# Kernel optimization log

Measured on AMD Instinct MI355X. Metric: run time of the kernel, lower is better.

Reference implementation:

```python
import jax, jax.numpy as jnp
import numpy as np

BN_EPS = 1e-5


def setup_inputs() -> dict:
    key = jax.random.key(0)
    ks = jax.random.split(key, 12)
    N, K, C_IN, C_OUT = 50000, 16, 128, 128
    C2 = 2 * C_OUT
    return {
        "features": jax.random.normal(ks[0], (N, C_IN), dtype=jnp.float32),
        "neighbor_idx": jax.random.randint(ks[1], (N, K), 0, N, dtype=jnp.int64),
        "W1": jax.random.normal(ks[2], (C_IN, C2), dtype=jnp.float32) * 0.05,
        "b1": jax.random.normal(ks[3], (C2,), dtype=jnp.float32) * 0.05,
        "gamma": jax.random.uniform(ks[4], (C2,), dtype=jnp.float32, minval=0.5, maxval=1.5),
        "beta": jax.random.normal(ks[5], (C2,), dtype=jnp.float32) * 0.05,
        "run_mean": jax.random.normal(ks[6], (C2,), dtype=jnp.float32) * 0.05,
        "run_var": jax.random.uniform(ks[7], (C2,), dtype=jnp.float32, minval=0.5, maxval=1.5),
        "Ws": jax.random.normal(ks[8], (C2, C2), dtype=jnp.float32) * 0.05,
        "Wm": jax.random.normal(ks[9], (C2, C_OUT), dtype=jnp.float32) * 0.05,
        "bm": jax.random.normal(ks[10], (C_OUT,), dtype=jnp.float32) * 0.05,
    }


def reference(features, neighbor_idx, W1, b1, gamma, beta, run_mean, run_var, Ws, Wm, bm):
    # mlp1: Linear + ReLU (no BN)
    x = jax.nn.relu(features @ W1 + b1)                     # (N, 2C)
    # gather_neighbour: irregular index_select
    g = x[neighbor_idx]                                     # (N, k, 2C)
    # BatchNorm1d over channel dim (inference semantics, running stats)
    inv = gamma * jax.lax.rsqrt(run_var + BN_EPS)
    g = (g - run_mean) * inv + beta                         # (N, k, 2C)
    # AttentivePooling: per-neighbor score linear (no bias), softmax over k
    scores = jax.nn.softmax(g @ Ws, axis=1)                 # (N, k, 2C)
    feat = jnp.sum(scores * g, axis=1)                      # (N, 2C)
    return feat @ Wm + bm                                   # (N, C_out)
```

## Files before the change

kernel.cpp:

```cpp
#include <hip/hip_runtime.h>
#include <cstddef>

#define C_IN  128
#define C2    256
#define C_OUT 128
#define KNBR  16

typedef unsigned short u16;
typedef __attribute__((ext_vector_type(8))) short bf16x8;
typedef __attribute__((ext_vector_type(4))) float f32x4;

__device__ __forceinline__ float bf2f(u16 h) {
    return __uint_as_float(((unsigned int)h) << 16);
}
__device__ __forceinline__ u16 f2bf(float x) {
    unsigned int u = __float_as_uint(x);
    return (u16)((u + 0x7fffu + ((u >> 16) & 1u)) >> 16);
}

__global__ void prep_k(const float* __restrict__ W1, const float* __restrict__ Ws,
                       const float* __restrict__ Wm, u16* __restrict__ W1t,
                       u16* __restrict__ Wst, u16* __restrict__ Wmt)
{
    const int n = blockIdx.x, t = threadIdx.x;
    if (blockIdx.y == 0) {
        if (t < 128) W1t[n * 128 + t] = f2bf(W1[t * 256 + n]);
    } else if (blockIdx.y == 1) {
        Wst[n * 256 + t] = f2bf(Ws[t * 256 + n]);
    } else {
        if (n < 128) Wmt[n * 256 + t] = f2bf(Wm[t * 128 + n]);
    }
}

__global__ __launch_bounds__(256)
void mlp_k(const float* __restrict__ F, const u16* __restrict__ W1t,
           const u16* __restrict__ Wst,
           const float* __restrict__ bias, const float* __restrict__ gamma,
           const float* __restrict__ beta, const float* __restrict__ mean,
           const float* __restrict__ var,
           u16* __restrict__ packed, int N)
{
    __shared__ u16 As[128][136];
    __shared__ u16 Bs[128][72];
    __shared__ u16 xs[128][264];

    const int tid = threadIdx.x;
    const int w = tid >> 6, l = tid & 63, q = l >> 4, r = l & 15;
    const int wm = w & 1, wn = w >> 1;
    const int m0 = blockIdx.x * 128;

    #pragma unroll
    for (int i = 0; i < 16; i++) {
        int idx = tid + i * 256;
        int row = idx >> 5, c4 = (idx & 31) * 4;
        int gm = m0 + row;
        float4 v = make_float4(0.f, 0.f, 0.f, 0.f);
        if (gm < N) v = *(const float4*)(F + (size_t)gm * C_IN + c4);
        ushort4 h;
        h.x = f2bf(v.x); h.y = f2bf(v.y); h.z = f2bf(v.z); h.w = f2bf(v.w);
        *(ushort4*)&As[row][c4] = h;
    }

    #pragma unroll 1
    for (int nh = 0; nh < 2; nh++) {
        f32x4 acc[4][4] = {};
        #pragma unroll 1
        for (int k0 = 0; k0 < C_IN; k0 += 64) {
            __syncthreads();
            #pragma unroll
            for (int i = 0; i < 4; i++) {
                int idx = tid + i * 256;
                int row = idx >> 3, g = (idx & 7) * 8;
                *(uint4*)&Bs[row][g] = *(const uint4*)(
                    W1t + (size_t)(nh * 128 + row) * C_IN + k0 + g);
            }
            __syncthreads();
            #pragma unroll
            for (int h = 0; h < 2; h++) {
                bf16x8 af[4], bfr[4];
                #pragma unroll
                for (int i = 0; i < 4; i++)
                    af[i] = *(const bf16x8*)&As[wm * 64 + i * 16 + r][k0 + h * 32 + q * 8];
                #pragma unroll
                for (int j = 0; j < 4; j++)
                    bfr[j] = *(const bf16x8*)&Bs[wn * 64 + j * 16 + r][h * 32 + q * 8];
                #pragma unroll
                for (int i = 0; i < 4; i++)
                    #pragma unroll
                    for (int j = 0; j < 4; j++)
                        acc[i][j] = __builtin_amdgcn_mfma_f32_16x16x32_bf16(
                            af[i], bfr[j], acc[i][j], 0, 0, 0);
            }
        }
        #pragma unroll
        for (int j = 0; j < 4; j++) {
            const int ch = nh * 128 + wn * 64 + j * 16 + r;
            const float bi = bias[ch], be = beta[ch], mu = mean[ch];
            const float iv = gamma[ch] * rsqrtf(var[ch] + 1e-5f);
            #pragma unroll
            for (int i = 0; i < 4; i++) {
                const int mb = wm * 64 + i * 16 + q * 4;
                #pragma unroll
                for (int p = 0; p < 4; p++) {
                    const int ml = mb + p;
                    float x = fmaxf(acc[i][j][p] + bi, 0.f);
                    x = (x - mu) * iv + be;
                    u16 hx = f2bf(x);
                    xs[ml][ch] = hx;
                    if (m0 + ml < N)
                        packed[(size_t)(m0 + ml) * 512 + 256 + ch] = hx;
                }
            }
        }
    }

    #pragma unroll 1
    for (int nh = 0; nh < 2; nh++) {
        f32x4 acc[4][4] = {};
        #pragma unroll 1
        for (int k0 = 0; k0 < C2; k0 += 64) {
            __syncthreads();
            #pragma unroll
            for (int i = 0; i < 4; i++) {
                int idx = tid + i * 256;
                int row = idx >> 3, g = (idx & 7) * 8;
                *(uint4*)&Bs[row][g] = *(const uint4*)(
                    Wst + (size_t)(nh * 128 + row) * C2 + k0 + g);
            }
            __syncthreads();
            #pragma unroll
            for (int h = 0; h < 2; h++) {
                bf16x8 af[4], bfr[4];
                #pragma unroll
                for (int i = 0; i < 4; i++)
                    af[i] = *(const bf16x8*)&xs[wm * 64 + i * 16 + r][k0 + h * 32 + q * 8];
                #pragma unroll
                for (int j = 0; j < 4; j++)
                    bfr[j] = *(const bf16x8*)&Bs[wn * 64 + j * 16 + r][h * 32 + q * 8];
                #pragma unroll
                for (int i = 0; i < 4; i++)
                    #pragma unroll
                    for (int j = 0; j < 4; j++)
                        acc[i][j] = __builtin_amdgcn_mfma_f32_16x16x32_bf16(
                            af[i], bfr[j], acc[i][j], 0, 0, 0);
            }
        }
        #pragma unroll
        for (int j = 0; j < 4; j++) {
            const int ch = nh * 128 + wn * 64 + j * 16 + r;
            #pragma unroll
            for (int i = 0; i < 4; i++) {
                const int mb = wm * 64 + i * 16 + q * 4;
                #pragma unroll
                for (int p = 0; p < 4; p++) {
                    const int ml = mb + p;
                    if (m0 + ml < N)
                        packed[(size_t)(m0 + ml) * 512 + ch] =
                            f2bf(__expf(acc[i][j][p]));
                }
            }
        }
    }
}

__global__ __launch_bounds__(256)
void out_gemm(const u16* __restrict__ A, const u16* __restrict__ Bt,
              const float* __restrict__ bias, float* __restrict__ Cf, int N)
{
    __shared__ u16 As[128][72];
    __shared__ u16 Bs[128][72];
    const int tid = threadIdx.x;
    const int w = tid >> 6, l = tid & 63, q = l >> 4, r = l & 15;
    const int wm = w & 1, wn = w >> 1;
    const int m0 = blockIdx.x * 128;

    f32x4 acc[4][4] = {};

    #pragma unroll 1
    for (int k0 = 0; k0 < C2; k0 += 64) {
        #pragma unroll
        for (int i = 0; i < 4; i++) {
            int idx = tid + i * 256;
            int row = idx >> 3, g = (idx & 7) * 8;
            int gm = m0 + row;
            uint4 v = make_uint4(0u, 0u, 0u, 0u);
            if (gm < N) v = *(const uint4*)(A + (size_t)gm * C2 + k0 + g);
            *(uint4*)&As[row][g] = v;
            *(uint4*)&Bs[row][g] = *(const uint4*)(
                Bt + (size_t)row * C2 + k0 + g);
        }
        __syncthreads();
        #pragma unroll
        for (int h = 0; h < 2; h++) {
            bf16x8 af[4], bfr[4];
            #pragma unroll
            for (int i = 0; i < 4; i++)
                af[i] = *(const bf16x8*)&As[wm * 64 + i * 16 + r][h * 32 + q * 8];
            #pragma unroll
            for (int j = 0; j < 4; j++)
                bfr[j] = *(const bf16x8*)&Bs[wn * 64 + j * 16 + r][h * 32 + q * 8];
            #pragma unroll
            for (int i = 0; i < 4; i++)
                #pragma unroll
                for (int j = 0; j < 4; j++)
                    acc[i][j] = __builtin_amdgcn_mfma_f32_16x16x32_bf16(
                        af[i], bfr[j], acc[i][j], 0, 0, 0);
        }
        __syncthreads();
    }

    #pragma unroll
    for (int j = 0; j < 4; j++) {
        const int ch = wn * 64 + j * 16 + r;
        const float bo = bias[ch];
        #pragma unroll
        for (int i = 0; i < 4; i++) {
            const int mb = m0 + wm * 64 + i * 16 + q * 4;
            #pragma unroll
            for (int p = 0; p < 4; p++) {
                const int m = mb + p;
                if (m < N) Cf[(size_t)m * C_OUT + ch] = acc[i][j][p] + bo;
            }
        }
    }
}

__global__ __launch_bounds__(256)
void gather_k(const u16* __restrict__ packed, const int* __restrict__ nidx,
              u16* __restrict__ featb, int N)
{
    __shared__ int rows[4 * KNBR];
    const int tid = threadIdx.x;
    const int p0 = blockIdx.x * 4;

    if (tid < 4 * KNBR) {
        int n = p0 + (tid >> 4);
        rows[tid] = (n < N) ? nidx[n * KNBR + (tid & 15)] : 0;
    }
    __syncthreads();

    const int w = tid >> 6;
    const int l = tid & 63;
    const int p = p0 + w;
    if (p >= N) return;

    ushort4 eh[KNBR], xh[KNBR];
    #pragma unroll
    for (int k = 0; k < KNBR; k++) {
        const size_t base = (size_t)rows[w * KNBR + k] * 512;
        eh[k] = *(const ushort4*)(packed + base + l * 4);
        xh[k] = *(const ushort4*)(packed + base + 256 + l * 4);
    }

    float d0 = 0.f, d1 = 0.f, d2 = 0.f, d3 = 0.f;
    float u0 = 0.f, u1 = 0.f, u2 = 0.f, u3 = 0.f;
    #pragma unroll
    for (int k = 0; k < KNBR; k++) {
        float e0 = bf2f(eh[k].x), e1 = bf2f(eh[k].y);
        float e2 = bf2f(eh[k].z), e3 = bf2f(eh[k].w);
        d0 += e0; d1 += e1; d2 += e2; d3 += e3;
        u0 = fmaf(e0, bf2f(xh[k].x), u0);
        u1 = fmaf(e1, bf2f(xh[k].y), u1);
        u2 = fmaf(e2, bf2f(xh[k].z), u2);
        u3 = fmaf(e3, bf2f(xh[k].w), u3);
    }
    ushort4 o;
    o.x = f2bf(u0 / d0); o.y = f2bf(u1 / d1);
    o.z = f2bf(u2 / d2); o.w = f2bf(u3 / d3);
    *(ushort4*)(featb + (size_t)p * C2 + l * 4) = o;
}

extern "C" void kernel_launch(void* const* d_in, const int* in_sizes, int n_in,
                              void* d_out, int out_size, void* d_ws, size_t ws_size,
                              hipStream_t stream)
{
    const float* features = (const float*)d_in[0];
    const int*   nidx     = (const int*)d_in[1];
    const float* W1       = (const float*)d_in[2];
    const float* b1       = (const float*)d_in[3];
    const float* gamma    = (const float*)d_in[4];
    const float* beta     = (const float*)d_in[5];
    const float* mean     = (const float*)d_in[6];
    const float* var      = (const float*)d_in[7];
    const float* Ws       = (const float*)d_in[8];
    const float* Wm       = (const float*)d_in[9];
    const float* bm       = (const float*)d_in[10];
    float* out = (float*)d_out;

    const int N = in_sizes[0] / C_IN;

    u16* packed = (u16*)d_ws;
    u16* W1t    = packed + (size_t)N * 512;
    u16* Wst    = W1t + 256 * 128;
    u16* Wmt    = Wst + 256 * 256;
    u16* featb = (u16*)d_out;

    prep_k<<<dim3(256, 3), 256, 0, stream>>>(W1, Ws, Wm, W1t, Wst, Wmt);

    const int MT = (N + 127) / 128;

    mlp_k<<<MT, 256, 0, stream>>>(features, W1t, Wst, b1, gamma, beta,
                                  mean, var, packed, N);
    gather_k<<<(N + 3) / 4, 256, 0, stream>>>(packed, nidx, featb, N);
    out_gemm<<<MT, 256, 0, stream>>>(featb, Wmt, bm, out, N);
}
```

Before: 268.2 us.

## Fuse neighbor gather-pool with output GEMM and shrink MLP tiles to 64 rows

Merges the gather/softmax-pool kernel and the output GEMM into one kernel that pools 64 points into shared memory and then multiplies by Wm with register-prefetched weights. This removes the round trip of the pooled bf16 features through global memory and one launch. The MLP kernel moves to 64-row tiles, giving more blocks and less shared memory per block, and stages its outputs through shared memory so global stores are coalesced 16-byte writes. The cost is fewer points in flight per wave during the gather, which may expose more gather latency, and a separately pipelined GEMM stage in each block.

After: 399.1 us. +48.8%, slower.

```diff
diff --git a/kernel.cpp b/kernel.cpp
--- a/kernel.cpp
+++ b/kernel.cpp
@@ -34,23 +34,22 @@
 
 __global__ __launch_bounds__(256)
 void mlp_k(const float* __restrict__ F, const u16* __restrict__ W1t,
-           const u16* __restrict__ Wst,
-           const float* __restrict__ bias, const float* __restrict__ gamma,
-           const float* __restrict__ beta, const float* __restrict__ mean,
-           const float* __restrict__ var,
+           const u16* __restrict__ Wst, const float* __restrict__ bias,
+           const float* __restrict__ gamma, const float* __restrict__ beta,
+           const float* __restrict__ mean, const float* __restrict__ var,
            u16* __restrict__ packed, int N)
 {
-    __shared__ u16 As[128][136];
+    __shared__ u16 As[64][136];
     __shared__ u16 Bs[128][72];
-    __shared__ u16 xs[128][264];
+    __shared__ u16 xs[64][272];
 
     const int tid = threadIdx.x;
     const int w = tid >> 6, l = tid & 63, q = l >> 4, r = l & 15;
     const int wm = w & 1, wn = w >> 1;
-    const int m0 = blockIdx.x * 128;
-
-    #pragma unroll
-    for (int i = 0; i < 16; i++) {
+    const int m0 = blockIdx.x * 64;
+
+    #pragma unroll
+    for (int i = 0; i < 8; i++) {
         int idx = tid + i * 256;
         int row = idx >> 5, c4 = (idx & 31) * 4;
         int gm = m0 + row;
@@ -61,9 +60,9 @@
         *(ushort4*)&As[row][c4] = h;
     }
 
+    f32x4 acc1[2][2][4] = {};
     #pragma unroll 1
     for (int nh = 0; nh < 2; nh++) {
-        f32x4 acc[4][4] = {};
         #pragma unroll 1
         for (int k0 = 0; k0 < C_IN; k0 += 64) {
             __syncthreads();
@@ -77,46 +76,52 @@
             __syncthreads();
             #pragma unroll
             for (int h = 0; h < 2; h++) {
-                bf16x8 af[4], bfr[4];
-                #pragma unroll
-                for (int i = 0; i < 4; i++)
-                    af[i] = *(const bf16x8*)&As[wm * 64 + i * 16 + r][k0 + h * 32 + q * 8];
+                bf16x8 af[2], bfr[4];
+                #pragma unroll
+                for (int i = 0; i < 2; i++)
+                    af[i] = *(const bf16x8*)&As[wm * 32 + i * 16 + r][k0 + h * 32 + q * 8];
                 #pragma unroll
                 for (int j = 0; j < 4; j++)
                     bfr[j] = *(const bf16x8*)&Bs[wn * 64 + j * 16 + r][h * 32 + q * 8];
                 #pragma unroll
-                for (int i = 0; i < 4; i++)
+                for (int i = 0; i < 2; i++)
                     #pragma unroll
                     for (int j = 0; j < 4; j++)
-                        acc[i][j] = __builtin_amdgcn_mfma_f32_16x16x32_bf16(
-                            af[i], bfr[j], acc[i][j], 0, 0, 0);
-            }
-        }
+                        acc1[nh][i][j] = __builtin_amdgcn_mfma_f32_16x16x32_bf16(
+                            af[i], bfr[j], acc1[nh][i][j], 0, 0, 0);
+            }
+        }
+    }
+    #pragma unroll
+    for (int nh = 0; nh < 2; nh++)
         #pragma unroll
         for (int j = 0; j < 4; j++) {
             const int ch = nh * 128 + wn * 64 + j * 16 + r;
             const float bi = bias[ch], be = beta[ch], mu = mean[ch];
             const float iv = gamma[ch] * rsqrtf(var[ch] + 1e-5f);
             #pragma unroll
-            for (int i = 0; i < 4; i++) {
-                const int mb = wm * 64 + i * 16 + q * 4;
+            for (int i = 0; i < 2; i++)
                 #pragma unroll
                 for (int p = 0; p < 4; p++) {
-                    const int ml = mb + p;
-                    float x = fmaxf(acc[i][j][p] + bi, 0.f);
+                    const int ml = wm * 32 + i * 16 + q * 4 + p;
+                    float x = fmaxf(acc1[nh][i][j][p] + bi, 0.f);
                     x = (x - mu) * iv + be;
-                    u16 hx = f2bf(x);
-                    xs[ml][ch] = hx;
-                    if (m0 + ml < N)
-                        packed[(size_t)(m0 + ml) * 512 + 256 + ch] = hx;
+                    xs[ml][ch] = f2bf(x);
                 }
-            }
-        }
-    }
-
+        }
+    __syncthreads();
+    #pragma unroll
+    for (int i = 0; i < 8; i++) {
+        int idx = tid + i * 256;
+        int row = idx >> 5, g = (idx & 31) * 8;
+        if (m0 + row < N)
+            *(uint4*)(packed + (size_t)(m0 + row) * 512 + 256 + g) =
+                *(const uint4*)&xs[row][g];
+    }
+
+    f32x4 acc2[2][2][4] = {};
     #pragma unroll 1
     for (int nh = 0; nh < 2; nh++) {
-        f32x4 acc[4][4] = {};
         #pragma unroll 1
         for (int k0 = 0; k0 < C2; k0 += 64) {
             __syncthreads();
@@ -130,144 +135,152 @@
             __syncthreads();
             #pragma unroll
             for (int h = 0; h < 2; h++) {
-                bf16x8 af[4], bfr[4];
-                #pragma unroll
-                for (int i = 0; i < 4; i++)
-                    af[i] = *(const bf16x8*)&xs[wm * 64 + i * 16 + r][k0 + h * 32 + q * 8];
+                bf16x8 af[2], bfr[4];
+                #pragma unroll
+                for (int i = 0; i < 2; i++)
+                    af[i] = *(const bf16x8*)&xs[wm * 32 + i * 16 + r][k0 + h * 32 + q * 8];
                 #pragma unroll
                 for (int j = 0; j < 4; j++)
                     bfr[j] = *(const bf16x8*)&Bs[wn * 64 + j * 16 + r][h * 32 + q * 8];
                 #pragma unroll
-                for (int i = 0; i < 4; i++)
+                for (int i = 0; i < 2; i++)
                     #pragma unroll
                     for (int j = 0; j < 4; j++)
-                        acc[i][j] = __builtin_amdgcn_mfma_f32_16x16x32_bf16(
-                            af[i], bfr[j], acc[i][j], 0, 0, 0);
-            }
-        }
+                        acc2[nh][i][j] = __builtin_amdgcn_mfma_f32_16x16x32_bf16(
+                            af[i], bfr[j], acc2[nh][i][j], 0, 0, 0);
+            }
+        }
+    }
+    __syncthreads();
+    #pragma unroll
+    for (int nh = 0; nh < 2; nh++)
         #pragma unroll
         for (int j = 0; j < 4; j++) {
             const int ch = nh * 128 + wn * 64 + j * 16 + r;
             #pragma unroll
-            for (int i = 0; i < 4; i++) {
-                const int mb = wm * 64 + i * 16 + q * 4;
+            for (int i = 0; i < 2; i++)
                 #pragma unroll
                 for (int p = 0; p < 4; p++) {
-                    const int ml = mb + p;
-                    if (m0 + ml < N)
-                        packed[(size_t)(m0 + ml) * 512 + ch] =
-                            f2bf(__expf(acc[i][j][p]));
+                    const int ml = wm * 32 + i * 16 + q * 4 + p;
+                    xs[ml][ch] = f2bf(__expf(acc2[nh][i][j][p]));
                 }
-            }
-        }
-    }
-}
-
-__global__ __launch_bounds__(256)
-void out_gemm(const u16* __restrict__ A, const u16* __restrict__ Bt,
-              const float* __restrict__ bias, float* __restrict__ Cf, int N)
+        }
+    __syncthreads();
+    #pragma unroll
+    for (int i = 0; i < 8; i++) {
+        int idx = tid + i * 256;
+        int row = idx >> 5, g = (idx & 31) * 8;
+        if (m0 + row < N)
+            *(uint4*)(packed + (size_t)(m0 + row) * 512 + g) =
+                *(const uint4*)&xs[row][g];
+    }
+}
+
+__global__ __launch_bounds__(256, 4)
+void gout_k(const u16* __restrict__ packed, const int* __restrict__ nidx,
+            const u16* __restrict__ Wmt, const float* __restrict__ bm,
+            float* __restrict__ out, int N)
 {
-    __shared__ u16 As[128][72];
-    __shared__ u16 Bs[128][72];
+    __shared__ int rows[64 * KNBR];
+    __shared__ u16 fs[64][272];
     const int tid = threadIdx.x;
     const int w = tid >> 6, l = tid & 63, q = l >> 4, r = l & 15;
     const int wm = w & 1, wn = w >> 1;
-    const int m0 = blockIdx.x * 128;
-
-    f32x4 acc[4][4] = {};
+    const int m0 = blockIdx.x * 64;
+
+    {
+        int gi = m0 * KNBR + tid * 4;
+        int4 v;
+        if (gi + 3 < N * KNBR) v = *(const int4*)(nidx + gi);
+        else {
+            v.x = (gi + 0 < N * KNBR) ? nidx[gi + 0] : 0;
+            v.y = (gi + 1 < N * KNBR) ? nidx[gi + 1] : 0;
+            v.z = (gi + 2 < N * KNBR) ? nidx[gi + 2] : 0;
+            v.w = (gi + 3 < N * KNBR) ? nidx[gi + 3] : 0;
+        }
+        *(int4*)&rows[tid * 4] = v;
+    }
+    __syncthreads();
 
     #pragma unroll 1
-    for (int k0 = 0; k0 < C2; k0 += 64) {
-        #pragma unroll
-        for (int i = 0; i < 4; i++) {
-            int idx = tid + i * 256;
-            int row = idx >> 3, g = (idx & 7) * 8;
-            int gm = m0 + row;
-            uint4 v = make_uint4(0u, 0u, 0u, 0u);
-            if (gm < N) v = *(const uint4*)(A + (size_t)gm * C2 + k0 + g);
-            *(uint4*)&As[row][g] = v;
-            *(uint4*)&Bs[row][g] = *(const uint4*)(
-                Bt + (size_t)row * C2 + k0 + g);
-        }
-        __syncthreads();
-        #pragma unroll
-        for (int h = 0; h < 2; h++) {
-            bf16x8 af[4], bfr[4];
-            #pragma unroll
-            for (int i = 0; i < 4; i++)
-                af[i] = *(const bf16x8*)&As[wm * 64 + i * 16 + r][h * 32 + q * 8];
+    for (int pi = 0; pi < 16; pi++) {
+        const int lp = w * 16 + pi;
+        ushort4 eh[KNBR], xh[KNBR];
+        #pragma unroll
+        for (int k = 0; k < KNBR; k++) {
+            const size_t base = (size_t)rows[lp * KNBR + k] * 512;
+            eh[k] = *(const ushort4*)(packed + base + l * 4);
+            xh[k] = *(const ushort4*)(packed + base + 256 + l * 4);
+        }
+        float d0 = 0.f, d1 = 0.f, d2 = 0.f, d3 = 0.f;
+        float u0 = 0.f, u1 = 0.f, u2 = 0.f, u3 = 0.f;
+        #pragma unroll
+        for (int k = 0; k < KNBR; k++) {
+            float e0 = bf2f(eh[k].x), e1 = bf2f(eh[k].y);
+            float e2 = bf2f(eh[k].z), e3 = bf2f(eh[k].w);
+            d0 += e0; d1 += e1; d2 += e2; d3 += e3;
+            u0 = fmaf(e0, bf2f(xh[k].x), u0);
+            u1 = fmaf(e1, bf2f(xh[k].y), u1);
+            u2 = fmaf(e2, bf2f(xh[k].z), u2);
+            u3 = fmaf(e3, bf2f(xh[k].w), u3);
+        }
+        ushort4 o;
+        o.x = f2bf(u0 / d0); o.y = f2bf(u1 / d1);
+        o.z = f2bf(u2 / d2); o.w = f2bf(u3 / d3);
+        *(ushort4*)&fs[lp][l * 4] = o;
+    }
+    __syncthreads();
+
+    f32x4 acc[2][4] = {};
+    uint4 bcur[4], bnxt[4];
+    #pragma unroll
+    for (int j = 0; j < 4; j++)
+        bcur[j] = *(const uint4*)(Wmt + (size_t)(wn * 64 + j * 16 + r) * C2 + q * 8);
+    #pragma unroll 1
+    for (int ks = 0; ks < 8; ks++) {
+        if (ks < 7) {
             #pragma unroll
             for (int j = 0; j < 4; j++)
-                bfr[j] = *(const bf16x8*)&Bs[wn * 64 + j * 16 + r][h * 32 + q * 8];
-            #pragma unroll
-            for (int i = 0; i < 4; i++)
-                #pragma unroll
-                for (int j = 0; j < 4; j++)
-                    acc[i][j] = __builtin_amdgcn_mfma_f32_16x16x32_bf16(
-                        af[i], bfr[j], acc[i][j], 0, 0, 0);
-        }
-        __syncthreads();
-    }
-
+                bnxt[j] = *(const uint4*)(
+                    Wmt + (size_t)(wn * 64 + j * 16 + r) * C2 + (ks + 1) * 32 + q * 8);
+        }
+        bf16x8 af[2];
+        #pragma unroll
+        for (int i = 0; i < 2; i++)
+            af[i] = *(const bf16x8*)&fs[wm * 32 + i * 16 + r][ks * 32 + q * 8];
+        #pragma unroll
+        for (int i = 0; i < 2; i++)
+            #pragma unroll
+            for (int j = 0; j < 4; j++)
+                acc[i][j] = __builtin_amdgcn_mfma_f32_16x16x32_bf16(
+                    af[i], *(const bf16x8*)&bcur[j], acc[i][j], 0, 0, 0);
+        #pragma unroll
+        for (int j = 0; j < 4; j++) bcur[j] = bnxt[j];
+    }
+    __syncthreads();
+
+    float* fsf = (float*)&fs[0][0];
     #pragma unroll
     for (int j = 0; j < 4; j++) {
         const int ch = wn * 64 + j * 16 + r;
-        const float bo = bias[ch];
-        #pragma unroll
-        for (int i = 0; i < 4; i++) {
-            const int mb = m0 + wm * 64 + i * 16 + q * 4;
+        const float bo = bm[ch];
+        #pragma unroll
+        for (int i = 0; i < 2; i++)
             #pragma unroll
             for (int p = 0; p < 4; p++) {
-                const int m = mb + p;
-                if (m < N) Cf[(size_t)m * C_OUT + ch] = acc[i][j][p] + bo;
-            }
-        }
-    }
-}
-
-__global__ __launch_bounds__(256)
-void gather_k(const u16* __restrict__ packed, const int* __restrict__ nidx,
-              u16* __restrict__ featb, int N)
-{
-    __shared__ int rows[4 * KNBR];
-    const int tid = threadIdx.x;
-    const int p0 = blockIdx.x * 4;
-
-    if (tid < 4 * KNBR) {
-        int n = p0 + (tid >> 4);
-        rows[tid] = (n < N) ? nidx[n * KNBR + (tid & 15)] : 0;
-    }
-    __syncthreads();
-
-    const int w = tid >> 6;
-    const int l = tid & 63;
-    const int p = p0 + w;
-    if (p >= N) return;
-
-    ushort4 eh[KNBR], xh[KNBR];
-    #pragma unroll
-    for (int k = 0; k < KNBR; k++) {
-        const size_t base = (size_t)rows[w * KNBR + k] * 512;
-        eh[k] = *(const ushort4*)(packed + base + l * 4);
-        xh[k] = *(const ushort4*)(packed + base + 256 + l * 4);
-    }
-
-    float d0 = 0.f, d1 = 0.f, d2 = 0.f, d3 = 0.f;
-    float u0 = 0.f, u1 = 0.f, u2 = 0.f, u3 = 0.f;
-    #pragma unroll
-    for (int k = 0; k < KNBR; k++) {
-        float e0 = bf2f(eh[k].x), e1 = bf2f(eh[k].y);
-        float e2 = bf2f(eh[k].z), e3 = bf2f(eh[k].w);
-        d0 += e0; d1 += e1; d2 += e2; d3 += e3;
-        u0 = fmaf(e0, bf2f(xh[k].x), u0);
-        u1 = fmaf(e1, bf2f(xh[k].y), u1);
-        u2 = fmaf(e2, bf2f(xh[k].z), u2);
-        u3 = fmaf(e3, bf2f(xh[k].w), u3);
-    }
-    ushort4 o;
-    o.x = f2bf(u0 / d0); o.y = f2bf(u1 / d1);
-    o.z = f2bf(u2 / d2); o.w = f2bf(u3 / d3);
-    *(ushort4*)(featb + (size_t)p * C2 + l * 4) = o;
+                const int ml = wm * 32 + i * 16 + q * 4 + p;
+                fsf[ml * C_OUT + ch] = acc[i][j][p] + bo;
+            }
+    }
+    __syncthreads();
+    #pragma unroll
+    for (int i = 0; i < 8; i++) {
+        int idx = tid + i * 256;
+        int row = idx >> 5, c4 = (idx & 31) * 4;
+        if (m0 + row < N)
+            *(float4*)(out + (size_t)(m0 + row) * C_OUT + c4) =
+                *(const float4*)&fsf[row * C_OUT + c4];
+    }
 }
 
 extern "C" void kernel_launch(void* const* d_in, const int* in_sizes, int n_in,
@@ -293,14 +306,12 @@
     u16* W1t    = packed + (size_t)N * 512;
     u16* Wst    = W1t + 256 * 128;
     u16* Wmt    = Wst + 256 * 256;
-    u16* featb = (u16*)d_out;
 
     prep_k<<<dim3(256, 3), 256, 0, stream>>>(W1, Ws, Wm, W1t, Wst, Wmt);
 
-    const int MT = (N + 127) / 128;
+    const int MT = (N + 63) / 64;
 
     mlp_k<<<MT, 256, 0, stream>>>(features, W1t, Wst, b1, gamma, beta,
                                   mean, var, packed, N);
-    gather_k<<<(N + 3) / 4, 256, 0, stream>>>(packed, nidx, featb, N);
-    out_gemm<<<MT, 256, 0, stream>>>(featb, Wmt, bm, out, N);
-}
+    gout_k<<<MT, 256, 0, stream>>>(packed, nidx, Wmt, bm, out, N);
+}
```
